# Optimization experiments

Hardware: AMD Instinct MI355X
Metric: run time of the kernel (lower is better)

The kernel has to match this reference:

```python
import jax, jax.numpy as jnp
import numpy as np

N, D, O, V, E, C = 100000, 128, 128, 3, 400000, 2

def setup_inputs() -> dict:
    key = jax.random.key(0)
    ks = jax.random.split(key, 32)
    s = 0.05
    inp = {
        'features': jax.random.normal(ks[0], (N, D), jnp.float32),
        'edge_index': jax.random.randint(ks[1], (V, 2, E), 0, N, jnp.int32),
        'edge_weight': jax.random.uniform(ks[2], (V, E), jnp.float32),
        # per-view RelationAggregator (single relation each)
        'rel_w': jax.random.normal(ks[3], (V, D, O)) * s,
        'rel_b': jnp.zeros((V, O)),
        'gate_w': jax.random.normal(ks[4], (V, O, O)) * s,
        'gate_b': jnp.zeros((V, O)),
        # LabelAwareAttention
        'la_w1': jax.random.normal(ks[5], (C, D, D // 2)) * s,
        'la_b1': jnp.zeros((C, D // 2)),
        'la_w2': jax.random.normal(ks[6], (C, D // 2)) * s,
        'la_b2': jnp.zeros((C,)),
        'pred_w': jax.random.normal(ks[7], (D, C)) * s,
        'pred_b': jnp.zeros((C,)),
        'att_bias': jnp.float32(0.1),
        # ViewLevelAttention
        'view_pref': jax.random.normal(ks[8], (V, O)),
        'va_w1': jax.random.normal(ks[9], (O, O // 2)) * s,
        'va_b1': jnp.zeros((O // 2,)),
        'va_w2': jax.random.normal(ks[10], (O // 2,)) * s,
        'va_b2': jnp.float32(0.0),
        # linear heads
        'ft_w': jax.random.normal(ks[11], (D, O)) * s,
        'ft_b': jnp.zeros((O,)),
        'sl_w': jax.random.normal(ks[12], (D, O)) * s,
        'sl_b': jnp.zeros((O,)),
        'fus_w': jax.random.normal(ks[13], (2 * O, O)) * s,
        'fus_b': jnp.zeros((O,)),
        'ln_g': jnp.ones((O,)),
        'ln_beta': jnp.zeros((O,)),
    }
    return inp


def _aggregate_view(features, ei, ew, w, b, gw, gb):
    # gather -> linear -> edge weight -> scatter-add (fused segment_sum)
    msg = (features[ei[0]] @ w + b) * ew[:, None]          # [E, O]
    agg = jax.ops.segment_sum(msg, ei[1], num_segments=N)  # [N, O]
    # relation_weight_net: softmax over 1 relation == 1.0 (identity)
    gate = jax.nn.sigmoid(agg @ gw + gb)
    return gate * agg


def reference(features, edge_index, edge_weight, rel_w, rel_b, gate_w, gate_b,
              la_w1, la_b1, la_w2, la_b2, pred_w, pred_b, att_bias,
              view_pref, va_w1, va_b1, va_w2, va_b2,
              ft_w, ft_b, sl_w, sl_b, fus_w, fus_b, ln_g, ln_beta):
    # --- label-aware attention ---
    class_probs = jax.nn.softmax(features @ pred_w + pred_b, axis=-1)        # [N, C]
    h = jax.nn.relu(jnp.einsum('nd,cdk->nck', features, la_w1) + la_b1)      # [N, C, D/2]
    scores = jax.nn.sigmoid(jnp.einsum('nck,ck->nc', h, la_w2) + la_b2)      # [N, C]
    node_att = jnp.sum(scores * class_probs, axis=-1) + att_bias             # [N]

    # --- per-view relation aggregation ---
    views = jax.vmap(_aggregate_view, in_axes=(None, 0, 0, 0, 0, 0, 0))(
        features, edge_index, edge_weight, rel_w, rel_b, gate_w, gate_b)     # [V, N, O]

    # --- view-level attention ---
    pe = views * view_pref[:, None, :]                                       # [V, N, O]
    vh = jax.nn.relu(jnp.einsum('vno,ok->vnk', pe, va_w1) + va_b1)           # [V, N, O/2]
    vscore = jnp.einsum('vnk,k->vn', vh, va_w2) + va_b2                      # [V, N]
    v_att = jax.nn.softmax(vscore, axis=0)                                   # over views
    combined = jnp.sum(views * v_att[..., None], axis=0)                     # [N, O]

    # --- fusion (dropout in eval mode == identity) ---
    self_out = features @ sl_w + sl_b
    transformed = features @ ft_w + ft_b
    weighted = combined * node_att[:, None]
    fused = jax.nn.relu(jnp.concatenate([self_out, weighted], axis=-1) @ fus_w + fus_b)
    out = fused + transformed

    mu = jnp.mean(out, axis=-1, keepdims=True)
    var = jnp.mean(jnp.square(out - mu), axis=-1, keepdims=True)
    out = (out - mu) / jnp.sqrt(var + 1e-5) * ln_g + ln_beta
    return out, class_probs
```

## Files before the change

### kernel.cpp

```cpp
#include <hip/hip_runtime.h>

#define N_ 100000
#define D_ 128
#define O_ 128
#define V_ 3
#define E_ 400000
#define NB_SCAN 98
#define EGRID 1563
#define MB 32
#define NBLK (N_ / MB)
#define LDA 136

#define PRE_CVT  6250
#define PRE_PREW (PRE_CVT + 64)
#define PRE_PREP (PRE_PREW + 617)
#define PRE_TOT  (PRE_PREP + 3 * EGRID)

typedef unsigned short u16;
typedef __attribute__((ext_vector_type(8))) short bf16x8;
typedef __attribute__((ext_vector_type(4))) float f32x4;

#define MFMA16x16x32 __builtin_amdgcn_mfma_f32_16x16x32_bf16

#define P_RELB  0
#define P_GATEB 384
#define P_VP    768
#define P_VAB1  1152
#define P_VAW2  1216
#define P_VAB2  1280
#define P_LAB1  1281
#define P_LAW2  1409
#define P_LAB2  1537
#define P_PREDB 1539
#define P_ATTB  1541
#define P_FTB   1542
#define P_LNG   1670
#define P_LNB   1798
#define P_PREDW 1926
#define P_TOTAL 2182

__device__ __forceinline__ float b2f(u16 u) {
    union { float f; unsigned int i; } x; x.i = ((unsigned int)u) << 16; return x.f;
}
__device__ __forceinline__ float blo(unsigned int u) {
    union { float f; unsigned int i; } x; x.i = u << 16; return x.f;
}
__device__ __forceinline__ float bhi(unsigned int u) {
    union { float f; unsigned int i; } x; x.i = u & 0xffff0000u; return x.f;
}
__device__ __forceinline__ u16 f2b(float f) {
    union { float f; unsigned int i; } x; x.f = f;
    unsigned int r = x.i + 0x7FFFu + ((x.i >> 16) & 1u);
    return (u16)(r >> 16);
}

template<int F32> __device__ __forceinline__ float LD(const void* p, size_t i) {
    if (F32) return ((const float*)p)[i];
    return b2f(((const u16*)p)[i]);
}

__global__ void k_detect(const u16* __restrict__ feat, int* __restrict__ flag) {
    int t = threadIdx.x;
    u16 a = feat[2 * t], b = feat[2 * t + 128];
    int zeros = (a == 0 ? 1 : 0) + (b == 0 ? 1 : 0);
    float va = b2f(a), vb = b2f(b);
    int bad = (!(va > -128.f && va < 128.f) ? 1 : 0) +
              (!(vb > -128.f && vb < 128.f) ? 1 : 0);
    #pragma unroll
    for (int s = 1; s <= 32; s <<= 1) {
        bad += __shfl_xor(bad, s);
        zeros += __shfl_xor(zeros, s);
    }
    if (t == 0) flag[0] = (bad >= 16 || zeros >= 64) ? 1 : 0;
}

__device__ __forceinline__ void cvt_body_f32(int b, const void* feat,
                                             u16* __restrict__ featB) {
    size_t idx = (size_t)b * 256 + threadIdx.x;
    const float4* fp = (const float4*)feat;
    float4 a = fp[idx * 2], c = fp[idx * 2 + 1];
    uint4 u;
    u.x = (unsigned)f2b(a.x) | ((unsigned)f2b(a.y) << 16);
    u.y = (unsigned)f2b(a.z) | ((unsigned)f2b(a.w) << 16);
    u.z = (unsigned)f2b(c.x) | ((unsigned)f2b(c.y) << 16);
    u.w = (unsigned)f2b(c.z) | ((unsigned)f2b(c.w) << 16);
    ((uint4*)featB)[idx] = u;
}

template<int F32>
__device__ __forceinline__ void prew_body(int b, const void* sl_w, const void* sl_b,
                                          const void* fus_w, const void* fus_b,
                                          u16* __restrict__ W1T, float* __restrict__ b1) {
    int gid = b * 256 + threadIdx.x;
    int d = gid >> 7, o = gid & 127;
    float acc = 0.f;
    for (int k = 0; k < 128; ++k)
        acc += LD<F32>(sl_w, d * 128 + k) * LD<F32>(fus_w, k * 128 + o);
    W1T[o * 128 + d] = f2b(acc);
    if (gid < 128) {
        float accb = 0.f;
        for (int k = 0; k < 128; ++k)
            accb += LD<F32>(sl_b, k) * LD<F32>(fus_w, k * 128 + gid);
        b1[gid] = accb + LD<F32>(fus_b, gid);
    }
}

template<int F32>
__device__ __forceinline__ void prep_body(int b,
        const void* rel_w, const void* gate_w, const void* va_w1, const void* fus_w,
        const void* ft_w, const void* la_w1,
        const void* rel_b, const void* gate_b, const void* vpref,
        const void* va_b1, const void* va_w2, const void* va_b2,
        const void* la_b1, const void* la_w2, const void* la_b2,
        const void* pred_b, const void* att_bias, const void* ft_b,
        const void* ln_g, const void* ln_beta, const void* pred_w,
        u16* __restrict__ relT, u16* __restrict__ gateT, u16* __restrict__ vaT,
        u16* __restrict__ fus2T, u16* __restrict__ ftT, u16* __restrict__ laT,
        float* __restrict__ P) {
    int id = b * 256 + threadIdx.x;
    if (id < 49152) {
        int v = id >> 14, r = id & 16383, o = r >> 7, d = r & 127;
        relT[id] = f2b(LD<F32>(rel_w, (size_t)v * 16384 + d * 128 + o));
    } else if (id < 98304) {
        int t = id - 49152, v = t >> 14, r = t & 16383, o = r >> 7, d = r & 127;
        gateT[t] = f2b(LD<F32>(gate_w, (size_t)v * 16384 + d * 128 + o));
    } else if (id < 106496) {
        int t = id - 98304, n = t >> 7, k = t & 127;
        vaT[t] = f2b(LD<F32>(va_w1, k * 64 + n));
    } else if (id < 122880) {
        int t = id - 106496, n = t >> 7, k = t & 127;
        fus2T[t] = f2b(LD<F32>(fus_w, (128 + k) * 128 + n));
    } else if (id < 139264) {
        int t = id - 122880, o = t >> 7, d = t & 127;
        ftT[t] = f2b(LD<F32>(ft_w, d * 128 + o));
    } else if (id < 155648) {
        int t = id - 139264, n = t >> 7, d = t & 127;
        int c = n >> 6, j = n & 63;
        laT[t] = f2b(LD<F32>(la_w1, c * 8192 + d * 64 + j));
    } else if (id < 155648 + P_TOTAL) {
        int t = id - 155648;
        float val;
        if      (t < P_GATEB) val = LD<F32>(rel_b, t);
        else if (t < P_VP)    val = LD<F32>(gate_b, t - P_GATEB);
        else if (t < P_VAB1)  val = LD<F32>(vpref, t - P_VP);
        else if (t < P_VAW2)  val = LD<F32>(va_b1, t - P_VAB1);
        else if (t < P_VAB2)  val = LD<F32>(va_w2, t - P_VAW2);
        else if (t < P_LAB1)  val = LD<F32>(va_b2, 0);
        else if (t < P_LAW2)  val = LD<F32>(la_b1, t - P_LAB1);
        else if (t < P_LAB2)  val = LD<F32>(la_w2, t - P_LAW2);
        else if (t < P_PREDB) val = LD<F32>(la_b2, t - P_LAB2);
        else if (t < P_ATTB)  val = LD<F32>(pred_b, t - P_PREDB);
        else if (t < P_FTB)   val = LD<F32>(att_bias, 0);
        else if (t < P_LNG)   val = LD<F32>(ft_b, t - P_FTB);
        else if (t < P_LNB)   val = LD<F32>(ln_g, t - P_LNG);
        else if (t < P_PREDW) val = LD<F32>(ln_beta, t - P_LNB);
        else                  val = LD<F32>(pred_w, t - P_PREDW);
        P[t] = val;
    }
}

__global__ __launch_bounds__(256) void k_preC(const int* __restrict__ flag,
        const void* feat, u16* __restrict__ featB,
        const void* sl_w, const void* sl_b, const void* fus_w, const void* fus_b,
        u16* __restrict__ W1T, float* __restrict__ b1,
        const void* rel_w, const void* gate_w, const void* va_w1,
        const void* ft_w, const void* la_w1,
        const void* rel_b, const void* gate_b, const void* vpref,
        const void* va_b1, const void* va_w2, const void* va_b2,
        const void* la_b1, const void* la_w2, const void* la_b2,
        const void* pred_b, const void* att_bias, const void* ft_b,
        const void* ln_g, const void* ln_beta, const void* pred_w,
        u16* __restrict__ relT, u16* __restrict__ gateT, u16* __restrict__ vaT,
        u16* __restrict__ fus2T, u16* __restrict__ ftT, u16* __restrict__ laT,
        float* __restrict__ P,
        const int* __restrict__ ei, int* __restrict__ cur3) {
    int b = blockIdx.x;
    if (b < PRE_CVT) {
        if (flag[0]) cvt_body_f32(b, feat, featB);
    } else if (b < PRE_PREW) {
        if (flag[0]) prew_body<1>(b - PRE_CVT, sl_w, sl_b, fus_w, fus_b, W1T, b1);
        else         prew_body<0>(b - PRE_CVT, sl_w, sl_b, fus_w, fus_b, W1T, b1);
    } else if (b < PRE_PREP) {
        if (flag[0]) prep_body<1>(b - PRE_PREW, rel_w, gate_w, va_w1, fus_w, ft_w, la_w1,
                                  rel_b, gate_b, vpref, va_b1, va_w2, va_b2,
                                  la_b1, la_w2, la_b2, pred_b, att_bias, ft_b,
                                  ln_g, ln_beta, pred_w, relT, gateT, vaT, fus2T, ftT, laT, P);
        else         prep_body<0>(b - PRE_PREW, rel_w, gate_w, va_w1, fus_w, ft_w, la_w1,
                                  rel_b, gate_b, vpref, va_b1, va_w2, va_b2,
                                  la_b1, la_w2, la_b2, pred_b, att_bias, ft_b,
                                  ln_g, ln_beta, pred_w, relT, gateT, vaT, fus2T, ftT, laT, P);
    } else {
        int b2 = b - PRE_PREP;
        int v = b2 / EGRID;
        int e = (b2 % EGRID) * 256 + threadIdx.x;
        if (e < E_) atomicAdd(&cur3[v * N_ + ei[(size_t)v * 2 * E_ + E_ + e]], 1);
    }
}

__global__ __launch_bounds__(256) void k_scan_bsum(const int* __restrict__ cur3,
                                                   int* __restrict__ bsum) {
    __shared__ int red[256];
    const int v = blockIdx.x / NB_SCAN, b = blockIdx.x % NB_SCAN, tid = threadIdx.x;
    const int base = b * 1024;
    const int* counts = cur3 + v * N_;
    int s = 0;
    for (int i = tid; i < 1024; i += 256) {
        int idx = base + i;
        s += (idx < N_) ? counts[idx] : 0;
    }
    red[tid] = s;
    __syncthreads();
    for (int st = 128; st >= 1; st >>= 1) {
        if (tid < st) red[tid] += red[tid + st];
        __syncthreads();
    }
    if (tid == 0) bsum[v * 128 + b] = red[0];
}

__global__ __launch_bounds__(256) void k_scan_write(int* __restrict__ cur3,
                                                    const int* __restrict__ bsum,
                                                    int* __restrict__ offs3) {
    __shared__ int lsum[256];
    __shared__ int bs_s[128];
    const int v = blockIdx.x / NB_SCAN, b = blockIdx.x % NB_SCAN, tid = threadIdx.x;
    const int base = b * 1024;
    int* counts = cur3 + v * N_;
    int* offs   = offs3 + v * N_;
    if (tid < 128) bs_s[tid] = (tid < b) ? bsum[v * 128 + tid] : 0;
    int c[4]; int s = 0;
    #pragma unroll
    for (int k = 0; k < 4; ++k) {
        int idx = base + tid * 4 + k;
        c[k] = (idx < N_) ? counts[idx] : 0;
        s += c[k];
    }
    lsum[tid] = s;
    __syncthreads();
    for (int st = 1; st < 256; st <<= 1) {
        int t = (tid >= st) ? lsum[tid - st] : 0;
        __syncthreads();
        lsum[tid] += t;
        __syncthreads();
    }
    for (int st = 64; st >= 1; st >>= 1) {
        if (tid < st) bs_s[tid] += bs_s[tid + st];
        __syncthreads();
    }
    int off = bs_s[0] + lsum[tid] - s;
    #pragma unroll
    for (int k = 0; k < 4; ++k) {
        int idx = base + tid * 4 + k;
        if (idx < N_) { offs[idx] = off; counts[idx] = off; }
        off += c[k];
    }
}

template<int F32>
__device__ __forceinline__ void place_body(const int* __restrict__ ei, const void* ew_all,
                                           int* __restrict__ cur3, int2* __restrict__ srcw3) {
    int v = blockIdx.x / EGRID;
    int e = (blockIdx.x % EGRID) * 256 + threadIdx.x;
    if (e < E_) {
        int dst = ei[(size_t)v * 2 * E_ + E_ + e];
        int src = ei[(size_t)v * 2 * E_ + e];
        float w = LD<F32>(ew_all, (size_t)v * E_ + e);
        int pos = atomicAdd(&cur3[v * N_ + dst], 1);
        int2 sw; sw.x = src; sw.y = __float_as_int(w);
        srcw3[(size_t)v * E_ + pos] = sw;
    }
}
__global__ __launch_bounds__(256) void k_place(const int* __restrict__ flag,
                                               const int* __restrict__ ei, const void* ew,
                                               int* __restrict__ cur3, int2* __restrict__ srcw3) {
    if (flag[0]) place_body<1>(ei, ew, cur3, srcw3);
    else         place_body<0>(ei, ew, cur3, srcw3);
}

__global__ __launch_bounds__(768, 6) void k_fused(const int* __restrict__ flag,
        const void* feat, const u16* __restrict__ featB_,
        const int2* __restrict__ srcw3,
        const int* __restrict__ offs3, const int* __restrict__ ends3,
        const u16* __restrict__ relT, const u16* __restrict__ gateT,
        const u16* __restrict__ vaT, const u16* __restrict__ W1T,
        const u16* __restrict__ fus2T, const u16* __restrict__ ftT,
        const u16* __restrict__ laT,
        const float* __restrict__ b1, const float* __restrict__ P,
        void* __restrict__ d_out) {
    const int f32 = flag[0];
    const u16* __restrict__ fb = f32 ? featB_ : (const u16*)feat;

    __shared__ __align__(16) u16 xA[MB * LDA];
    __shared__ __align__(16) u16 zbuf[3][MB * LDA];
    __shared__ __align__(16) float Fbuf[MB * 128];
    __shared__ float vp3_s[3][128];
    __shared__ float redL[4][MB];
    __shared__ float redv[3][4][MB];
    __shared__ float wsn3[3][MB];
    __shared__ float aw_s[MB][3];
    __shared__ float natt_s[MB];
    __shared__ float lg_s[MB][2];
    __shared__ float mrs_s[MB][2];
    __shared__ float vab1_s[64], vaw2_s[64];
    __shared__ float predw_s[256];
    __shared__ float b1_s[128], ftb_s[128], lng_s[128], lnb_s[128];

    const int tid = threadIdx.x;
    const int g   = tid >> 8;
    const int t256 = tid & 255;
    const int wid = t256 >> 6;
    const int L = t256 & 63, q = L >> 4, i = L & 15;
    const int nb = wid * 32;
    const int nodebase = blockIdx.x * MB;
    const int nl = t256 >> 5, l32 = t256 & 31, o4 = l32 * 4;
    const int gsub = t256 >> 4, l16 = tid & 15, o8 = l16 * 8;
    const f32x4 zz = {0.f, 0.f, 0.f, 0.f};

    auto ldf = [&](const u16* B, int row, int k0) -> bf16x8 {
        return *(const bf16x8*)&B[row * LDA + k0];
    };
    auto ldg = [&](const u16* B, int row, int k0) -> bf16x8 {
        return *(const bf16x8*)&B[row * 128 + k0];
    };
    auto gemm32 = [&](const u16* A, const u16* Bg, f32x4 acc[2][2]) {
        #pragma unroll
        for (int kk = 0; kk < 4; ++kk) {
            int k0 = q * 8 + kk * 32;
            bf16x8 a0 = ldf(A, i, k0);
            bf16x8 a1 = ldf(A, i + 16, k0);
            bf16x8 bb0 = ldg(Bg, nb + i, k0);
            bf16x8 bb1 = ldg(Bg, nb + 16 + i, k0);
            acc[0][0] = MFMA16x16x32(a0, bb0, acc[0][0], 0, 0, 0);
            acc[0][1] = MFMA16x16x32(a0, bb1, acc[0][1], 0, 0, 0);
            acc[1][0] = MFMA16x16x32(a1, bb0, acc[1][0], 0, 0, 0);
            acc[1][1] = MFMA16x16x32(a1, bb1, acc[1][1], 0, 0, 0);
        }
    };
    auto gather = [&]() {
        const int* offs = offs3 + g * N_;
        const int* ends = ends3 + g * N_;
        const int2* srcw = srcw3 + (size_t)g * E_;
        #pragma unroll
        for (int rep = 0; rep < 2; ++rep) {
            const int m = gsub + rep * 16;
            const int node = nodebase + m;
            float z0 = 0.f, z1 = 0.f, z2 = 0.f, z3 = 0.f;
            float z4 = 0.f, z5 = 0.f, z6 = 0.f, z7 = 0.f, ws = 0.f;
            int j = offs[node], jend = ends[node];
            while (j < jend) {
                int r = jend - j;
                int2 e0 = srcw[j];
                int2 e1, e2, e3;
                e1.x = 0; e1.y = 0; e2.x = 0; e2.y = 0; e3.x = 0; e3.y = 0;
                if (r > 1) e1 = srcw[j + 1];
                if (r > 2) e2 = srcw[j + 2];
                if (r > 3) e3 = srcw[j + 3];
                uint4 x0, x1, x2, x3;
                x1.x = x1.y = x1.z = x1.w = 0;
                x2.x = x2.y = x2.z = x2.w = 0;
                x3.x = x3.y = x3.z = x3.w = 0;
                x0 = *(const uint4*)&fb[(size_t)e0.x * 128 + o8];
                if (r > 1) x1 = *(const uint4*)&fb[(size_t)e1.x * 128 + o8];
                if (r > 2) x2 = *(const uint4*)&fb[(size_t)e2.x * 128 + o8];
                if (r > 3) x3 = *(const uint4*)&fb[(size_t)e3.x * 128 + o8];
                float w0 = __int_as_float(e0.y), w1 = __int_as_float(e1.y);
                float w2 = __int_as_float(e2.y), w3 = __int_as_float(e3.y);
                ws += w0 + w1 + w2 + w3;
                z0 += w0 * blo(x0.x) + w1 * blo(x1.x) + w2 * blo(x2.x) + w3 * blo(x3.x);
                z1 += w0 * bhi(x0.x) + w1 * bhi(x1.x) + w2 * bhi(x2.x) + w3 * bhi(x3.x);
                z2 += w0 * blo(x0.y) + w1 * blo(x1.y) + w2 * blo(x2.y) + w3 * blo(x3.y);
                z3 += w0 * bhi(x0.y) + w1 * bhi(x1.y) + w2 * bhi(x2.y) + w3 * bhi(x3.y);
                z4 += w0 * blo(x0.z) + w1 * blo(x1.z) + w2 * blo(x2.z) + w3 * blo(x3.z);
                z5 += w0 * bhi(x0.z) + w1 * bhi(x1.z) + w2 * bhi(x2.z) + w3 * bhi(x3.z);
                z6 += w0 * blo(x0.w) + w1 * blo(x1.w) + w2 * blo(x2.w) + w3 * blo(x3.w);
                z7 += w0 * bhi(x0.w) + w1 * bhi(x1.w) + w2 * bhi(x2.w) + w3 * bhi(x3.w);
                j += 4;
            }
            uint4 u;
            u.x = (unsigned)f2b(z0) | ((unsigned)f2b(z1) << 16);
            u.y = (unsigned)f2b(z2) | ((unsigned)f2b(z3) << 16);
            u.z = (unsigned)f2b(z4) | ((unsigned)f2b(z5) << 16);
            u.w = (unsigned)f2b(z6) | ((unsigned)f2b(z7) << 16);
            *(uint4*)&zbuf[g][m * LDA + o8] = u;
            if (l16 == 0) wsn3[g][m] = ws;
        }
    };

    if (tid < 512) {
        int m = tid >> 4, s = tid & 15;
        *(uint4*)&xA[m * LDA + s * 8] =
            *(const uint4*)&fb[(size_t)(nodebase + m) * 128 + s * 8];
    }
    if (tid < 64) { vab1_s[tid] = P[P_VAB1 + tid]; vaw2_s[tid] = P[P_VAW2 + tid]; }
    if (tid < 128) {
        b1_s[tid]  = b1[tid];
        ftb_s[tid] = P[P_FTB + tid];
        lng_s[tid] = P[P_LNG + tid];
        lnb_s[tid] = P[P_LNB + tid];
    }
    if (tid < 256) predw_s[tid] = P[P_PREDW + tid];
    if (tid >= 256 && tid < 640) {
        int t = tid - 256;
        vp3_s[t >> 7][t & 127] = P[P_VP + t];
    }
    gather();
    __syncthreads();

    f32x4 accA[2][2] = {{zz, zz}, {zz, zz}};
    gemm32(zbuf[g], relT + (size_t)g * 16384, accA);
    if (g == 0) {
        f32x4 accL[2][2] = {{zz, zz}, {zz, zz}};
        gemm32(xA, laT, accL);
        #pragma unroll
        for (int rep = 0; rep < 4; ++rep) {
            int m = rep * 8 + nl;
            float lg0 = 0.f, lg1 = 0.f;
            #pragma unroll
            for (int t = 0; t < 4; ++t) {
                float xv = b2f(xA[m * LDA + o4 + t]);
                lg0 += xv * predw_s[(o4 + t) * 2 + 0];
                lg1 += xv * predw_s[(o4 + t) * 2 + 1];
            }
            #pragma unroll
            for (int s = 1; s <= 16; s <<= 1) {
                lg0 += __shfl_xor(lg0, s);
                lg1 += __shfl_xor(lg1, s);
            }
            if (l32 == 0) { lg_s[m][0] = lg0; lg_s[m][1] = lg1; }
        }
        float la0 = P[P_LAB1 + nb + i],  la1 = P[P_LAB1 + nb + 16 + i];
        float lw0 = P[P_LAW2 + nb + i],  lw1 = P[P_LAW2 + nb + 16 + i];
        float partL[2][4];
        #pragma unroll
        for (int mt = 0; mt < 2; ++mt)
            #pragma unroll
            for (int r = 0; r < 4; ++r) {
                float h0 = fmaxf(accL[mt][0][r] + la0, 0.f);
                float h1 = fmaxf(accL[mt][1][r] + la1, 0.f);
                partL[mt][r] = h0 * lw0 + h1 * lw1;
            }
        #pragma unroll
        for (int s = 1; s <= 8; s <<= 1)
            #pragma unroll
            for (int mt = 0; mt < 2; ++mt)
                #pragma unroll
                for (int r = 0; r < 4; ++r)
                    partL[mt][r] += __shfl_xor(partL[mt][r], s);
        if (i == 0)
            #pragma unroll
            for (int mt = 0; mt < 2; ++mt)
                #pragma unroll
                for (int r = 0; r < 4; ++r)
                    redL[wid][mt * 16 + q * 4 + r] = partL[mt][r];
    }
    __syncthreads();

    {
        float rb0 = P[P_RELB + g * 128 + nb + i];
        float rb1 = P[P_RELB + g * 128 + nb + 16 + i];
        #pragma unroll
        for (int mt = 0; mt < 2; ++mt)
            #pragma unroll
            for (int nt = 0; nt < 2; ++nt) {
                float rb = nt ? rb1 : rb0;
                int col = nb + nt * 16 + i;
                #pragma unroll
                for (int r = 0; r < 4; ++r) {
                    int row = mt * 16 + q * 4 + r;
                    float a = accA[mt][nt][r] + wsn3[g][row] * rb;
                    accA[mt][nt][r] = a;
                    zbuf[g][row * LDA + col] = f2b(a);
                }
            }
    }
    if (tid < MB) {
        float c0 = redL[0][tid] + redL[1][tid] + P[P_LAB2 + 0];
        float c1 = redL[2][tid] + redL[3][tid] + P[P_LAB2 + 1];
        float s0 = 1.f / (1.f + __expf(-c0));
        float s1 = 1.f / (1.f + __expf(-c1));
        float l0 = lg_s[tid][0] + P[P_PREDB + 0];
        float l1 = lg_s[tid][1] + P[P_PREDB + 1];
        float mx = fmaxf(l0, l1);
        float e0 = __expf(l0 - mx), e1 = __expf(l1 - mx);
        float inv = 1.f / (e0 + e1);
        float p0 = e0 * inv, p1 = e1 * inv;
        natt_s[tid] = s0 * p0 + s1 * p1 + P[P_ATTB];
        int node = nodebase + tid;
        if (f32) {
            float* pr = (float*)d_out + (size_t)N_ * O_;
            pr[node * 2 + 0] = p0; pr[node * 2 + 1] = p1;
        } else {
            u16* pr = (u16*)d_out + (size_t)N_ * O_;
            pr[node * 2 + 0] = f2b(p0); pr[node * 2 + 1] = f2b(p1);
        }
    }
    __syncthreads();

    f32x4 acc2[2][2] = {{zz, zz}, {zz, zz}};
    gemm32(zbuf[g], gateT + (size_t)g * 16384, acc2);
    __syncthreads();

    {
        float gb0 = P[P_GATEB + g * 128 + nb + i];
        float gb1 = P[P_GATEB + g * 128 + nb + 16 + i];
        #pragma unroll
        for (int mt = 0; mt < 2; ++mt)
            #pragma unroll
            for (int nt = 0; nt < 2; ++nt) {
                float gb = nt ? gb1 : gb0;
                int col = nb + nt * 16 + i;
                #pragma unroll
                for (int r = 0; r < 4; ++r) {
                    int row = mt * 16 + q * 4 + r;
                    float gt = 1.f / (1.f + __expf(-(acc2[mt][nt][r] + gb)));
                    zbuf[g][row * LDA + col] = f2b(gt * accA[mt][nt][r]);
                }
            }
    }
    __syncthreads();

    {
        f32x4 accV[2] = {zz, zz};
        const int nbv = wid * 16, colv = nbv + i;
        #pragma unroll
        for (int kk = 0; kk < 4; ++kk) {
            int k0 = q * 8 + kk * 32;
            bf16x8 a0r = ldf(zbuf[g], i, k0);
            bf16x8 a1r = ldf(zbuf[g], i + 16, k0);
            bf16x8 a0, a1;
            #pragma unroll
            for (int e = 0; e < 8; ++e) {
                float vp = vp3_s[g][k0 + e];
                a0[e] = (short)f2b(b2f((u16)a0r[e]) * vp);
                a1[e] = (short)f2b(b2f((u16)a1r[e]) * vp);
            }
            bf16x8 bb = ldg(vaT, nbv + i, k0);
            accV[0] = MFMA16x16x32(a0, bb, accV[0], 0, 0, 0);
            accV[1] = MFMA16x16x32(a1, bb, accV[1], 0, 0, 0);
        }
        float part[2][4];
        #pragma unroll
        for (int mt = 0; mt < 2; ++mt)
            #pragma unroll
            for (int r = 0; r < 4; ++r) {
                float vh = fmaxf(accV[mt][r] + vab1_s[colv], 0.f);
                part[mt][r] = vh * vaw2_s[colv];
            }
        #pragma unroll
        for (int s = 1; s <= 8; s <<= 1)
            #pragma unroll
            for (int mt = 0; mt < 2; ++mt)
                #pragma unroll
                for (int r = 0; r < 4; ++r)
                    part[mt][r] += __shfl_xor(part[mt][r], s);
        if (i == 0)
            #pragma unroll
            for (int mt = 0; mt < 2; ++mt)
                #pragma unroll
                for (int r = 0; r < 4; ++r)
                    redv[g][wid][mt * 16 + q * 4 + r] = part[mt][r];
    }
    __syncthreads();

    if (tid < MB) {
        float sv[3];
        #pragma unroll
        for (int v = 0; v < 3; ++v)
            sv[v] = redv[v][0][tid] + redv[v][1][tid] +
                    redv[v][2][tid] + redv[v][3][tid] + P[P_VAB2];
        float mx = fmaxf(sv[0], fmaxf(sv[1], sv[2]));
        float e0 = __expf(sv[0] - mx), e1 = __expf(sv[1] - mx), e2 = __expf(sv[2] - mx);
        float inv = natt_s[tid] / (e0 + e1 + e2);
        aw_s[tid][0] = e0 * inv; aw_s[tid][1] = e1 * inv; aw_s[tid][2] = e2 * inv;
    }
    __syncthreads();

    for (int idx = tid; idx < MB * 128; idx += 768) {
        int row = idx >> 7, col = idx & 127;
        float w = aw_s[row][0] * b2f(zbuf[0][row * LDA + col]) +
                  aw_s[row][1] * b2f(zbuf[1][row * LDA + col]) +
                  aw_s[row][2] * b2f(zbuf[2][row * LDA + col]);
        zbuf[0][row * LDA + col] = f2b(w);
    }
    __syncthreads();

    float* F1 = (float*)&zbuf[1][0];
    f32x4 accG[2][2] = {{zz, zz}, {zz, zz}};
    if (g == 0) {
        gemm32(xA, W1T, accG);
        #pragma unroll
        for (int mt = 0; mt < 2; ++mt)
            #pragma unroll
            for (int nt = 0; nt < 2; ++nt)
                #pragma unroll
                for (int r = 0; r < 4; ++r)
                    F1[(mt * 16 + q * 4 + r) * 128 + nb + nt * 16 + i] = accG[mt][nt][r];
    } else if (g == 1) {
        gemm32(zbuf[0], fus2T, accG);
        #pragma unroll
        for (int mt = 0; mt < 2; ++mt)
            #pragma unroll
            for (int nt = 0; nt < 2; ++nt)
                #pragma unroll
                for (int r = 0; r < 4; ++r)
                    Fbuf[(mt * 16 + q * 4 + r) * 128 + nb + nt * 16 + i] = accG[mt][nt][r];
    } else {
        gemm32(xA, ftT, accG);
    }
    __syncthreads();

    float ov[2][2][4];
    if (g == 2) {
        float ps[2][4], pq[2][4];
        #pragma unroll
        for (int mt = 0; mt < 2; ++mt)
            #pragma unroll
            for (int r = 0; r < 4; ++r) { ps[mt][r] = 0.f; pq[mt][r] = 0.f; }
        #pragma unroll
        for (int mt = 0; mt < 2; ++mt)
            #pragma unroll
            for (int nt = 0; nt < 2; ++nt)
                #pragma unroll
                for (int r = 0; r < 4; ++r) {
                    int row = mt * 16 + q * 4 + r, col = nb + nt * 16 + i;
                    float o = fmaxf(F1[row * 128 + col] + Fbuf[row * 128 + col]
                                    + b1_s[col], 0.f)
                              + accG[mt][nt][r] + ftb_s[col];
                    ov[mt][nt][r] = o;
                    ps[mt][r] += o; pq[mt][r] += o * o;
                }
        #pragma unroll
        for (int s = 1; s <= 8; s <<= 1)
            #pragma unroll
            for (int mt = 0; mt < 2; ++mt)
                #pragma unroll
                for (int r = 0; r < 4; ++r) {
                    ps[mt][r] += __shfl_xor(ps[mt][r], s);
                    pq[mt][r] += __shfl_xor(pq[mt][r], s);
                }
        float* red2 = &redv[0][0][0];
        if (i == 0)
            #pragma unroll
            for (int mt = 0; mt < 2; ++mt)
                #pragma unroll
                for (int r = 0; r < 4; ++r) {
                    int row = mt * 16 + q * 4 + r;
                    red2[wid * 64 + row * 2 + 0] = ps[mt][r];
                    red2[wid * 64 + row * 2 + 1] = pq[mt][r];
                }
    }
    __syncthreads();

    if (tid < MB) {
        const float* red2 = &redv[0][0][0];
        float sm = red2[tid * 2] + red2[64 + tid * 2] +
                   red2[128 + tid * 2] + red2[192 + tid * 2];
        float sq = red2[tid * 2 + 1] + red2[64 + tid * 2 + 1] +
                   red2[128 + tid * 2 + 1] + red2[192 + tid * 2 + 1];
        float mu = sm * (1.f / 128.f);
        float var = sq * (1.f / 128.f) - mu * mu;
        mrs_s[tid][0] = mu; mrs_s[tid][1] = rsqrtf(var + 1e-5f);
    }
    __syncthreads();

    if (g == 2) {
        #pragma unroll
        for (int mt = 0; mt < 2; ++mt)
            #pragma unroll
            for (int nt = 0; nt < 2; ++nt)
                #pragma unroll
                for (int r = 0; r < 4; ++r) {
                    int row = mt * 16 + q * 4 + r, col = nb + nt * 16 + i;
                    float val = (ov[mt][nt][r] - mrs_s[row][0]) * mrs_s[row][1]
                                * lng_s[col] + lnb_s[col];
                    if (f32) Fbuf[row * 128 + col] = val;
                    else     ((u16*)Fbuf)[row * 128 + col] = f2b(val);
                }
    }
    __syncthreads();

    if (f32) {
        float* op = (float*)d_out + (size_t)nodebase * 128;
        for (int idx = tid; idx < 1024; idx += 768)
            ((float4*)op)[idx] = ((const float4*)Fbuf)[idx];
    } else {
        u16* op = (u16*)d_out + (size_t)nodebase * 128;
        if (tid < 512)
            ((uint4*)op)[tid] = ((const uint4*)Fbuf)[tid];
    }
}

extern "C" void kernel_launch(void* const* d_in, const int* in_sizes, int n_in,
                              void* d_out, int out_size, void* d_ws, size_t ws_size,
                              hipStream_t stream) {
    const void* feat     = d_in[0];
    const int*  ei       = (const int*)d_in[1];
    const void* ew       = d_in[2];
    const void* rel_w    = d_in[3];
    const void* rel_b    = d_in[4];
    const void* gate_w   = d_in[5];
    const void* gate_b   = d_in[6];
    const void* la_w1    = d_in[7];
    const void* la_b1    = d_in[8];
    const void* la_w2    = d_in[9];
    const void* la_b2    = d_in[10];
    const void* pred_w   = d_in[11];
    const void* pred_b   = d_in[12];
    const void* att_bias = d_in[13];
    const void* view_pref= d_in[14];
    const void* va_w1    = d_in[15];
    const void* va_b1    = d_in[16];
    const void* va_w2    = d_in[17];
    const void* va_b2    = d_in[18];
    const void* ft_w     = d_in[19];
    const void* ft_b     = d_in[20];
    const void* sl_w     = d_in[21];
    const void* sl_b     = d_in[22];
    const void* fus_w    = d_in[23];
    const void* fus_b    = d_in[24];
    const void* ln_g     = d_in[25];
    const void* ln_beta  = d_in[26];

    int*   flag  = (int*)d_ws;
    int*   offs3 = flag + 4;
    int*   cur3  = offs3 + 3 * N_;
    int2*  srcw3 = (int2*)(cur3 + 3 * N_);
    int*   bsum  = (int*)(srcw3 + 3 * E_);
    float* b1    = (float*)(bsum + 3 * 128);
    float* P     = b1 + 128;
    u16*   W1T   = (u16*)(P + 2304);
    u16*   relT  = W1T + 16384;
    u16*   gateT = relT + 3 * 16384;
    u16*   vaT   = gateT + 3 * 16384;
    u16*   fus2T = vaT + 8192;
    u16*   ftT   = fus2T + 16384;
    u16*   laT   = ftT + 16384;
    u16*   featB = laT + 16384;

    k_detect<<<1, 64, 0, stream>>>((const u16*)feat, flag);
    (void)hipMemsetAsync(cur3, 0, 3 * N_ * sizeof(int), stream);
    k_preC<<<PRE_TOT, 256, 0, stream>>>(flag, feat, featB,
                                        sl_w, sl_b, fus_w, fus_b, W1T, b1,
                                        rel_w, gate_w, va_w1, ft_w, la_w1,
                                        rel_b, gate_b, view_pref,
                                        va_b1, va_w2, va_b2,
                                        la_b1, la_w2, la_b2,
                                        pred_b, att_bias, ft_b, ln_g, ln_beta, pred_w,
                                        relT, gateT, vaT, fus2T, ftT, laT, P,
                                        ei, cur3);
    k_scan_bsum<<<3 * NB_SCAN, 256, 0, stream>>>(cur3, bsum);
    k_scan_write<<<3 * NB_SCAN, 256, 0, stream>>>(cur3, bsum, offs3);
    k_place<<<3 * EGRID, 256, 0, stream>>>(flag, ei, ew, cur3, srcw3);
    k_fused<<<NBLK, 768, 0, stream>>>(flag, feat, featB, srcw3, offs3, cur3,
                                      relT, gateT, vaT, W1T, fus2T, ftT, laT,
                                      b1, P, d_out);
}
```

Before: 544.2 us.

## Double node tile to 64 per block with aliased shared-memory buffers

Raises the fused kernel's node tile from 32 to 64, so each weight B-fragment loaded from global memory feeds four MFMA row tiles instead of two, halving per-node weight traffic. To fit the larger tile, the separate xA/zbuf/Fbuf shared arrays become one aliased buffer, several small parameter arrays are read straight from global memory, and LayerNorm is applied during the output store. Bounds checks handle the partial last block. This raises register pressure and shared-memory size per block, which may cut occupancy, especially with launch bounds still at (768,6).

New measurement: 610.6 us. 1.12x slower.

```diff
diff --git a/kernel.cpp b/kernel.cpp
--- a/kernel.cpp
+++ b/kernel.cpp
@@ -7,8 +7,8 @@
 #define E_ 400000
 #define NB_SCAN 98
 #define EGRID 1563
-#define MB 32
-#define NBLK (N_ / MB)
+#define MB 64
+#define NBLK 1563
 #define LDA 136
 
 #define PRE_CVT  6250
@@ -289,9 +289,7 @@
     const int f32 = flag[0];
     const u16* __restrict__ fb = f32 ? featB_ : (const u16*)feat;
 
-    __shared__ __align__(16) u16 xA[MB * LDA];
-    __shared__ __align__(16) u16 zbuf[3][MB * LDA];
-    __shared__ __align__(16) float Fbuf[MB * 128];
+    __shared__ __align__(16) u16 S[4 * MB * LDA];
     __shared__ float vp3_s[3][128];
     __shared__ float redL[4][MB];
     __shared__ float redv[3][4][MB];
@@ -300,9 +298,11 @@
     __shared__ float natt_s[MB];
     __shared__ float lg_s[MB][2];
     __shared__ float mrs_s[MB][2];
-    __shared__ float vab1_s[64], vaw2_s[64];
-    __shared__ float predw_s[256];
-    __shared__ float b1_s[128], ftb_s[128], lng_s[128], lnb_s[128];
+
+    u16* xA = S;
+    float* F1 = (float*)(S + 2 * MB * LDA);
+    float* F2 = (float*)S;
+    float* red2 = &redv[0][0][0];
 
     const int tid = threadIdx.x;
     const int g   = tid >> 8;
@@ -314,6 +314,7 @@
     const int nl = t256 >> 5, l32 = t256 & 31, o4 = l32 * 4;
     const int gsub = t256 >> 4, l16 = tid & 15, o8 = l16 * 8;
     const f32x4 zz = {0.f, 0.f, 0.f, 0.f};
+    u16* zc = S + (size_t)(1 + g) * MB * LDA;
 
     auto ldf = [&](const u16* B, int row, int k0) -> bf16x8 {
         return *(const bf16x8*)&B[row * LDA + k0];
@@ -321,18 +322,18 @@
     auto ldg = [&](const u16* B, int row, int k0) -> bf16x8 {
         return *(const bf16x8*)&B[row * 128 + k0];
     };
-    auto gemm32 = [&](const u16* A, const u16* Bg, f32x4 acc[2][2]) {
+    auto gemm64 = [&](const u16* A, const u16* Bg, f32x4 acc[4][2]) {
         #pragma unroll
         for (int kk = 0; kk < 4; ++kk) {
             int k0 = q * 8 + kk * 32;
-            bf16x8 a0 = ldf(A, i, k0);
-            bf16x8 a1 = ldf(A, i + 16, k0);
             bf16x8 bb0 = ldg(Bg, nb + i, k0);
             bf16x8 bb1 = ldg(Bg, nb + 16 + i, k0);
-            acc[0][0] = MFMA16x16x32(a0, bb0, acc[0][0], 0, 0, 0);
-            acc[0][1] = MFMA16x16x32(a0, bb1, acc[0][1], 0, 0, 0);
-            acc[1][0] = MFMA16x16x32(a1, bb0, acc[1][0], 0, 0, 0);
-            acc[1][1] = MFMA16x16x32(a1, bb1, acc[1][1], 0, 0, 0);
+            #pragma unroll
+            for (int mt = 0; mt < 4; ++mt) {
+                bf16x8 a = ldf(A, i + mt * 16, k0);
+                acc[mt][0] = MFMA16x16x32(a, bb0, acc[mt][0], 0, 0, 0);
+                acc[mt][1] = MFMA16x16x32(a, bb1, acc[mt][1], 0, 0, 0);
+            }
         }
     };
     auto gather = [&]() {
@@ -340,64 +341,60 @@
         const int* ends = ends3 + g * N_;
         const int2* srcw = srcw3 + (size_t)g * E_;
         #pragma unroll
-        for (int rep = 0; rep < 2; ++rep) {
+        for (int rep = 0; rep < 4; ++rep) {
             const int m = gsub + rep * 16;
             const int node = nodebase + m;
-            float z0 = 0.f, z1 = 0.f, z2 = 0.f, z3 = 0.f;
-            float z4 = 0.f, z5 = 0.f, z6 = 0.f, z7 = 0.f, ws = 0.f;
-            int j = offs[node], jend = ends[node];
-            while (j < jend) {
-                int r = jend - j;
-                int2 e0 = srcw[j];
-                int2 e1, e2, e3;
-                e1.x = 0; e1.y = 0; e2.x = 0; e2.y = 0; e3.x = 0; e3.y = 0;
-                if (r > 1) e1 = srcw[j + 1];
-                if (r > 2) e2 = srcw[j + 2];
-                if (r > 3) e3 = srcw[j + 3];
-                uint4 x0, x1, x2, x3;
-                x1.x = x1.y = x1.z = x1.w = 0;
-                x2.x = x2.y = x2.z = x2.w = 0;
-                x3.x = x3.y = x3.z = x3.w = 0;
-                x0 = *(const uint4*)&fb[(size_t)e0.x * 128 + o8];
-                if (r > 1) x1 = *(const uint4*)&fb[(size_t)e1.x * 128 + o8];
-                if (r > 2) x2 = *(const uint4*)&fb[(size_t)e2.x * 128 + o8];
-                if (r > 3) x3 = *(const uint4*)&fb[(size_t)e3.x * 128 + o8];
-                float w0 = __int_as_float(e0.y), w1 = __int_as_float(e1.y);
-                float w2 = __int_as_float(e2.y), w3 = __int_as_float(e3.y);
-                ws += w0 + w1 + w2 + w3;
-                z0 += w0 * blo(x0.x) + w1 * blo(x1.x) + w2 * blo(x2.x) + w3 * blo(x3.x);
-                z1 += w0 * bhi(x0.x) + w1 * bhi(x1.x) + w2 * bhi(x2.x) + w3 * bhi(x3.x);
-                z2 += w0 * blo(x0.y) + w1 * blo(x1.y) + w2 * blo(x2.y) + w3 * blo(x3.y);
-                z3 += w0 * bhi(x0.y) + w1 * bhi(x1.y) + w2 * bhi(x2.y) + w3 * bhi(x3.y);
-                z4 += w0 * blo(x0.z) + w1 * blo(x1.z) + w2 * blo(x2.z) + w3 * blo(x3.z);
-                z5 += w0 * bhi(x0.z) + w1 * bhi(x1.z) + w2 * bhi(x2.z) + w3 * bhi(x3.z);
-                z6 += w0 * blo(x0.w) + w1 * blo(x1.w) + w2 * blo(x2.w) + w3 * blo(x3.w);
-                z7 += w0 * bhi(x0.w) + w1 * bhi(x1.w) + w2 * bhi(x2.w) + w3 * bhi(x3.w);
-                j += 4;
-            }
-            uint4 u;
-            u.x = (unsigned)f2b(z0) | ((unsigned)f2b(z1) << 16);
-            u.y = (unsigned)f2b(z2) | ((unsigned)f2b(z3) << 16);
-            u.z = (unsigned)f2b(z4) | ((unsigned)f2b(z5) << 16);
-            u.w = (unsigned)f2b(z6) | ((unsigned)f2b(z7) << 16);
-            *(uint4*)&zbuf[g][m * LDA + o8] = u;
-            if (l16 == 0) wsn3[g][m] = ws;
+            if (node < N_) {
+                float z0 = 0.f, z1 = 0.f, z2 = 0.f, z3 = 0.f;
+                float z4 = 0.f, z5 = 0.f, z6 = 0.f, z7 = 0.f, ws = 0.f;
+                int j = offs[node], jend = ends[node];
+                while (j < jend) {
+                    int r = jend - j;
+                    int2 e0 = srcw[j];
+                    int2 e1, e2, e3;
+                    e1.x = 0; e1.y = 0; e2.x = 0; e2.y = 0; e3.x = 0; e3.y = 0;
+                    if (r > 1) e1 = srcw[j + 1];
+                    if (r > 2) e2 = srcw[j + 2];
+                    if (r > 3) e3 = srcw[j + 3];
+                    uint4 x0, x1, x2, x3;
+                    x1.x = x1.y = x1.z = x1.w = 0;
+                    x2.x = x2.y = x2.z = x2.w = 0;
+                    x3.x = x3.y = x3.z = x3.w = 0;
+                    x0 = *(const uint4*)&fb[(size_t)e0.x * 128 + o8];
+                    if (r > 1) x1 = *(const uint4*)&fb[(size_t)e1.x * 128 + o8];
+                    if (r > 2) x2 = *(const uint4*)&fb[(size_t)e2.x * 128 + o8];
+                    if (r > 3) x3 = *(const uint4*)&fb[(size_t)e3.x * 128 + o8];
+                    float w0 = __int_as_float(e0.y), w1 = __int_as_float(e1.y);
+                    float w2 = __int_as_float(e2.y), w3 = __int_as_float(e3.y);
+                    ws += w0 + w1 + w2 + w3;
+                    z0 += w0 * blo(x0.x) + w1 * blo(x1.x) + w2 * blo(x2.x) + w3 * blo(x3.x);
+                    z1 += w0 * bhi(x0.x) + w1 * bhi(x1.x) + w2 * bhi(x2.x) + w3 * bhi(x3.x);
+                    z2 += w0 * blo(x0.y) + w1 * blo(x1.y) + w2 * blo(x2.y) + w3 * blo(x3.y);
+                    z3 += w0 * bhi(x0.y) + w1 * bhi(x1.y) + w2 * bhi(x2.y) + w3 * bhi(x3.y);
+                    z4 += w0 * blo(x0.z) + w1 * blo(x1.z) + w2 * blo(x2.z) + w3 * blo(x3.z);
+                    z5 += w0 * bhi(x0.z) + w1 * bhi(x1.z) + w2 * bhi(x2.z) + w3 * bhi(x3.z);
+                    z6 += w0 * blo(x0.w) + w1 * blo(x1.w) + w2 * blo(x2.w) + w3 * blo(x3.w);
+                    z7 += w0 * bhi(x0.w) + w1 * bhi(x1.w) + w2 * bhi(x2.w) + w3 * bhi(x3.w);
+                    j += 4;
+                }
+                uint4 u;
+                u.x = (unsigned)f2b(z0) | ((unsigned)f2b(z1) << 16);
+                u.y = (unsigned)f2b(z2) | ((unsigned)f2b(z3) << 16);
+                u.z = (unsigned)f2b(z4) | ((unsigned)f2b(z5) << 16);
+                u.w = (unsigned)f2b(z6) | ((unsigned)f2b(z7) << 16);
+                *(uint4*)&zc[m * LDA + o8] = u;
+                if (l16 == 0) wsn3[g][m] = ws;
+            }
         }
     };
 
-    if (tid < 512) {
-        int m = tid >> 4, s = tid & 15;
-        *(uint4*)&xA[m * LDA + s * 8] =
-            *(const uint4*)&fb[(size_t)(nodebase + m) * 128 + s * 8];
-    }
-    if (tid < 64) { vab1_s[tid] = P[P_VAB1 + tid]; vaw2_s[tid] = P[P_VAW2 + tid]; }
-    if (tid < 128) {
-        b1_s[tid]  = b1[tid];
-        ftb_s[tid] = P[P_FTB + tid];
-        lng_s[tid] = P[P_LNG + tid];
-        lnb_s[tid] = P[P_LNB + tid];
-    }
-    if (tid < 256) predw_s[tid] = P[P_PREDW + tid];
+    for (int idx = tid; idx < MB * 16; idx += 768) {
+        int m = idx >> 4, s = idx & 15;
+        int node = nodebase + m;
+        uint4 u; u.x = 0; u.y = 0; u.z = 0; u.w = 0;
+        if (node < N_) u = *(const uint4*)&fb[(size_t)node * 128 + s * 8];
+        *(uint4*)&xA[m * LDA + s * 8] = u;
+    }
     if (tid >= 256 && tid < 640) {
         int t = tid - 256;
         vp3_s[t >> 7][t & 127] = P[P_VP + t];
@@ -405,20 +402,24 @@
     gather();
     __syncthreads();
 
-    f32x4 accA[2][2] = {{zz, zz}, {zz, zz}};
-    gemm32(zbuf[g], relT + (size_t)g * 16384, accA);
     if (g == 0) {
-        f32x4 accL[2][2] = {{zz, zz}, {zz, zz}};
-        gemm32(xA, laT, accL);
-        #pragma unroll
-        for (int rep = 0; rep < 4; ++rep) {
+        f32x4 accL[4][2] = {{zz, zz}, {zz, zz}, {zz, zz}, {zz, zz}};
+        gemm64(xA, laT, accL);
+        float pw[8];
+        #pragma unroll
+        for (int t = 0; t < 4; ++t) {
+            pw[2 * t]     = P[P_PREDW + (o4 + t) * 2];
+            pw[2 * t + 1] = P[P_PREDW + (o4 + t) * 2 + 1];
+        }
+        #pragma unroll
+        for (int rep = 0; rep < 8; ++rep) {
             int m = rep * 8 + nl;
             float lg0 = 0.f, lg1 = 0.f;
             #pragma unroll
             for (int t = 0; t < 4; ++t) {
                 float xv = b2f(xA[m * LDA + o4 + t]);
-                lg0 += xv * predw_s[(o4 + t) * 2 + 0];
-                lg1 += xv * predw_s[(o4 + t) * 2 + 1];
+                lg0 += xv * pw[2 * t];
+                lg1 += xv * pw[2 * t + 1];
             }
             #pragma unroll
             for (int s = 1; s <= 16; s <<= 1) {
@@ -429,36 +430,35 @@
         }
         float la0 = P[P_LAB1 + nb + i],  la1 = P[P_LAB1 + nb + 16 + i];
         float lw0 = P[P_LAW2 + nb + i],  lw1 = P[P_LAW2 + nb + 16 + i];
-        float partL[2][4];
-        #pragma unroll
-        for (int mt = 0; mt < 2; ++mt)
+        #pragma unroll
+        for (int mt = 0; mt < 4; ++mt) {
+            float partL[4];
             #pragma unroll
             for (int r = 0; r < 4; ++r) {
                 float h0 = fmaxf(accL[mt][0][r] + la0, 0.f);
                 float h1 = fmaxf(accL[mt][1][r] + la1, 0.f);
-                partL[mt][r] = h0 * lw0 + h1 * lw1;
-            }
-        #pragma unroll
-        for (int s = 1; s <= 8; s <<= 1)
-            #pragma unroll
-            for (int mt = 0; mt < 2; ++mt)
+                partL[r] = h0 * lw0 + h1 * lw1;
+            }
+            #pragma unroll
+            for (int s = 1; s <= 8; s <<= 1)
                 #pragma unroll
                 for (int r = 0; r < 4; ++r)
-                    partL[mt][r] += __shfl_xor(partL[mt][r], s);
-        if (i == 0)
-            #pragma unroll
-            for (int mt = 0; mt < 2; ++mt)
+                    partL[r] += __shfl_xor(partL[r], s);
+            if (i == 0)
                 #pragma unroll
                 for (int r = 0; r < 4; ++r)
-                    redL[wid][mt * 16 + q * 4 + r] = partL[mt][r];
-    }
+                    redL[wid][mt * 16 + q * 4 + r] = partL[r];
+        }
+    }
+    f32x4 accA[4][2] = {{zz, zz}, {zz, zz}, {zz, zz}, {zz, zz}};
+    gemm64(zc, relT + (size_t)g * 16384, accA);
     __syncthreads();
 
     {
         float rb0 = P[P_RELB + g * 128 + nb + i];
         float rb1 = P[P_RELB + g * 128 + nb + 16 + i];
         #pragma unroll
-        for (int mt = 0; mt < 2; ++mt)
+        for (int mt = 0; mt < 4; ++mt)
             #pragma unroll
             for (int nt = 0; nt < 2; ++nt) {
                 float rb = nt ? rb1 : rb0;
@@ -468,7 +468,7 @@
                     int row = mt * 16 + q * 4 + r;
                     float a = accA[mt][nt][r] + wsn3[g][row] * rb;
                     accA[mt][nt][r] = a;
-                    zbuf[g][row * LDA + col] = f2b(a);
+                    zc[row * LDA + col] = f2b(a);
                 }
             }
     }
@@ -485,25 +485,27 @@
         float p0 = e0 * inv, p1 = e1 * inv;
         natt_s[tid] = s0 * p0 + s1 * p1 + P[P_ATTB];
         int node = nodebase + tid;
-        if (f32) {
-            float* pr = (float*)d_out + (size_t)N_ * O_;
-            pr[node * 2 + 0] = p0; pr[node * 2 + 1] = p1;
-        } else {
-            u16* pr = (u16*)d_out + (size_t)N_ * O_;
-            pr[node * 2 + 0] = f2b(p0); pr[node * 2 + 1] = f2b(p1);
-        }
-    }
-    __syncthreads();
-
-    f32x4 acc2[2][2] = {{zz, zz}, {zz, zz}};
-    gemm32(zbuf[g], gateT + (size_t)g * 16384, acc2);
+        if (node < N_) {
+            if (f32) {
+                float* pr = (float*)d_out + (size_t)N_ * O_;
+                pr[node * 2 + 0] = p0; pr[node * 2 + 1] = p1;
+            } else {
+                u16* pr = (u16*)d_out + (size_t)N_ * O_;
+                pr[node * 2 + 0] = f2b(p0); pr[node * 2 + 1] = f2b(p1);
+            }
+        }
+    }
+    __syncthreads();
+
+    f32x4 acc2[4][2] = {{zz, zz}, {zz, zz}, {zz, zz}, {zz, zz}};
+    gemm64(zc, gateT + (size_t)g * 16384, acc2);
     __syncthreads();
 
     {
         float gb0 = P[P_GATEB + g * 128 + nb + i];
         float gb1 = P[P_GATEB + g * 128 + nb + 16 + i];
         #pragma unroll
-        for (int mt = 0; mt < 2; ++mt)
+        for (int mt = 0; mt < 4; ++mt)
             #pragma unroll
             for (int nt = 0; nt < 2; ++nt) {
                 float gb = nt ? gb1 : gb0;
@@ -512,52 +514,48 @@
                 for (int r = 0; r < 4; ++r) {
                     int row = mt * 16 + q * 4 + r;
                     float gt = 1.f / (1.f + __expf(-(acc2[mt][nt][r] + gb)));
-                    zbuf[g][row * LDA + col] = f2b(gt * accA[mt][nt][r]);
+                    zc[row * LDA + col] = f2b(gt * accA[mt][nt][r]);
                 }
             }
     }
     __syncthreads();
 
     {
-        f32x4 accV[2] = {zz, zz};
+        f32x4 accV[4] = {zz, zz, zz, zz};
         const int nbv = wid * 16, colv = nbv + i;
         #pragma unroll
         for (int kk = 0; kk < 4; ++kk) {
             int k0 = q * 8 + kk * 32;
-            bf16x8 a0r = ldf(zbuf[g], i, k0);
-            bf16x8 a1r = ldf(zbuf[g], i + 16, k0);
-            bf16x8 a0, a1;
-            #pragma unroll
-            for (int e = 0; e < 8; ++e) {
-                float vp = vp3_s[g][k0 + e];
-                a0[e] = (short)f2b(b2f((u16)a0r[e]) * vp);
-                a1[e] = (short)f2b(b2f((u16)a1r[e]) * vp);
-            }
             bf16x8 bb = ldg(vaT, nbv + i, k0);
-            accV[0] = MFMA16x16x32(a0, bb, accV[0], 0, 0, 0);
-            accV[1] = MFMA16x16x32(a1, bb, accV[1], 0, 0, 0);
-        }
-        float part[2][4];
-        #pragma unroll
-        for (int mt = 0; mt < 2; ++mt)
+            #pragma unroll
+            for (int mt = 0; mt < 4; ++mt) {
+                bf16x8 ar = ldf(zc, i + mt * 16, k0);
+                bf16x8 a;
+                #pragma unroll
+                for (int e = 0; e < 8; ++e)
+                    a[e] = (short)f2b(b2f((u16)ar[e]) * vp3_s[g][k0 + e]);
+                accV[mt] = MFMA16x16x32(a, bb, accV[mt], 0, 0, 0);
+            }
+        }
+        float vb1v = P[P_VAB1 + colv], vw2v = P[P_VAW2 + colv];
+        #pragma unroll
+        for (int mt = 0; mt < 4; ++mt) {
+            float part[4];
             #pragma unroll
             for (int r = 0; r < 4; ++r) {
-                float vh = fmaxf(accV[mt][r] + vab1_s[colv], 0.f);
-                part[mt][r] = vh * vaw2_s[colv];
-            }
-        #pragma unroll
-        for (int s = 1; s <= 8; s <<= 1)
-            #pragma unroll
-            for (int mt = 0; mt < 2; ++mt)
+                float vh = fmaxf(accV[mt][r] + vb1v, 0.f);
+                part[r] = vh * vw2v;
+            }
+            #pragma unroll
+            for (int s = 1; s <= 8; s <<= 1)
                 #pragma unroll
                 for (int r = 0; r < 4; ++r)
-                    part[mt][r] += __shfl_xor(part[mt][r], s);
-        if (i == 0)
-            #pragma unroll
-            for (int mt = 0; mt < 2; ++mt)
+                    part[r] += __shfl_xor(part[r], s);
+            if (i == 0)
                 #pragma unroll
                 for (int r = 0; r < 4; ++r)
-                    redv[g][wid][mt * 16 + q * 4 + r] = part[mt][r];
+                    redv[g][wid][mt * 16 + q * 4 + r] = part[r];
+        }
     }
     __syncthreads();
 
@@ -574,118 +572,118 @@
     }
     __syncthreads();
 
-    for (int idx = tid; idx < MB * 128; idx += 768) {
-        int row = idx >> 7, col = idx & 127;
-        float w = aw_s[row][0] * b2f(zbuf[0][row * LDA + col]) +
-                  aw_s[row][1] * b2f(zbuf[1][row * LDA + col]) +
-                  aw_s[row][2] * b2f(zbuf[2][row * LDA + col]);
-        zbuf[0][row * LDA + col] = f2b(w);
-    }
-    __syncthreads();
-
-    float* F1 = (float*)&zbuf[1][0];
-    f32x4 accG[2][2] = {{zz, zz}, {zz, zz}};
+    {
+        u16* z0p = S + MB * LDA;
+        u16* z1p = S + 2 * MB * LDA;
+        u16* z2p = S + 3 * MB * LDA;
+        for (int idx = tid; idx < MB * 128; idx += 768) {
+            int row = idx >> 7, col = idx & 127;
+            float w = aw_s[row][0] * b2f(z0p[row * LDA + col]) +
+                      aw_s[row][1] * b2f(z1p[row * LDA + col]) +
+                      aw_s[row][2] * b2f(z2p[row * LDA + col]);
+            z0p[row * LDA + col] = f2b(w);
+        }
+    }
+    __syncthreads();
+
+    f32x4 accG[4][2] = {{zz, zz}, {zz, zz}, {zz, zz}, {zz, zz}};
     if (g == 0) {
-        gemm32(xA, W1T, accG);
-        #pragma unroll
-        for (int mt = 0; mt < 2; ++mt)
+        gemm64(xA, W1T, accG);
+        #pragma unroll
+        for (int mt = 0; mt < 4; ++mt)
             #pragma unroll
             for (int nt = 0; nt < 2; ++nt)
                 #pragma unroll
                 for (int r = 0; r < 4; ++r)
                     F1[(mt * 16 + q * 4 + r) * 128 + nb + nt * 16 + i] = accG[mt][nt][r];
     } else if (g == 1) {
-        gemm32(zbuf[0], fus2T, accG);
-        #pragma unroll
-        for (int mt = 0; mt < 2; ++mt)
+        gemm64(S + MB * LDA, fus2T, accG);
+    } else {
+        gemm64(xA, ftT, accG);
+    }
+    __syncthreads();
+    if (g == 1) {
+        #pragma unroll
+        for (int mt = 0; mt < 4; ++mt)
             #pragma unroll
             for (int nt = 0; nt < 2; ++nt)
                 #pragma unroll
                 for (int r = 0; r < 4; ++r)
-                    Fbuf[(mt * 16 + q * 4 + r) * 128 + nb + nt * 16 + i] = accG[mt][nt][r];
-    } else {
-        gemm32(xA, ftT, accG);
-    }
-    __syncthreads();
-
-    float ov[2][2][4];
+                    F2[(mt * 16 + q * 4 + r) * 128 + nb + nt * 16 + i] = accG[mt][nt][r];
+    }
+    __syncthreads();
+
     if (g == 2) {
-        float ps[2][4], pq[2][4];
-        #pragma unroll
-        for (int mt = 0; mt < 2; ++mt)
-            #pragma unroll
-            for (int r = 0; r < 4; ++r) { ps[mt][r] = 0.f; pq[mt][r] = 0.f; }
-        #pragma unroll
-        for (int mt = 0; mt < 2; ++mt)
-            #pragma unroll
-            for (int nt = 0; nt < 2; ++nt)
+        float b1v0 = b1[nb + i], b1v1 = b1[nb + 16 + i];
+        float fb0 = P[P_FTB + nb + i], fb1 = P[P_FTB + nb + 16 + i];
+        #pragma unroll
+        for (int mt = 0; mt < 4; ++mt) {
+            float ps[4] = {0.f, 0.f, 0.f, 0.f}, pq[4] = {0.f, 0.f, 0.f, 0.f};
+            #pragma unroll
+            for (int nt = 0; nt < 2; ++nt) {
+                int col = nb + nt * 16 + i;
+                float bv = nt ? b1v1 : b1v0;
+                float fv = nt ? fb1 : fb0;
                 #pragma unroll
                 for (int r = 0; r < 4; ++r) {
-                    int row = mt * 16 + q * 4 + r, col = nb + nt * 16 + i;
-                    float o = fmaxf(F1[row * 128 + col] + Fbuf[row * 128 + col]
-                                    + b1_s[col], 0.f)
-                              + accG[mt][nt][r] + ftb_s[col];
-                    ov[mt][nt][r] = o;
-                    ps[mt][r] += o; pq[mt][r] += o * o;
+                    int rc = (mt * 16 + q * 4 + r) * 128 + col;
+                    float o = fmaxf(F1[rc] + F2[rc] + bv, 0.f) + accG[mt][nt][r] + fv;
+                    F1[rc] = o;
+                    ps[r] += o; pq[r] += o * o;
                 }
-        #pragma unroll
-        for (int s = 1; s <= 8; s <<= 1)
-            #pragma unroll
-            for (int mt = 0; mt < 2; ++mt)
+            }
+            #pragma unroll
+            for (int s = 1; s <= 8; s <<= 1)
                 #pragma unroll
                 for (int r = 0; r < 4; ++r) {
-                    ps[mt][r] += __shfl_xor(ps[mt][r], s);
-                    pq[mt][r] += __shfl_xor(pq[mt][r], s);
+                    ps[r] += __shfl_xor(ps[r], s);
+                    pq[r] += __shfl_xor(pq[r], s);
                 }
-        float* red2 = &redv[0][0][0];
-        if (i == 0)
-            #pragma unroll
-            for (int mt = 0; mt < 2; ++mt)
+            if (i == 0)
                 #pragma unroll
                 for (int r = 0; r < 4; ++r) {
                     int row = mt * 16 + q * 4 + r;
-                    red2[wid * 64 + row * 2 + 0] = ps[mt][r];
-                    red2[wid * 64 + row * 2 + 1] = pq[mt][r];
+                    red2[(wid * MB + row) * 2 + 0] = ps[r];
+                    red2[(wid * MB + row) * 2 + 1] = pq[r];
                 }
+        }
     }
     __syncthreads();
 
     if (tid < MB) {
-        const float* red2 = &redv[0][0][0];
-        float sm = red2[tid * 2] + red2[64 + tid * 2] +
-                   red2[128 + tid * 2] + red2[192 + tid * 2];
-        float sq = red2[tid * 2 + 1] + red2[64 + tid * 2 + 1] +
-                   red2[128 + tid * 2 + 1] + red2[192 + tid * 2 + 1];
+        float sm = red2[tid * 2]            + red2[(MB + tid) * 2] +
+                   red2[(2 * MB + tid) * 2] + red2[(3 * MB + tid) * 2];
+        float sq = red2[tid * 2 + 1]            + red2[(MB + tid) * 2 + 1] +
+                   red2[(2 * MB + tid) * 2 + 1] + red2[(3 * MB + tid) * 2 + 1];
         float mu = sm * (1.f / 128.f);
         float var = sq * (1.f / 128.f) - mu * mu;
         mrs_s[tid][0] = mu; mrs_s[tid][1] = rsqrtf(var + 1e-5f);
     }
     __syncthreads();
 
-    if (g == 2) {
-        #pragma unroll
-        for (int mt = 0; mt < 2; ++mt)
-            #pragma unroll
-            for (int nt = 0; nt < 2; ++nt)
-                #pragma unroll
-                for (int r = 0; r < 4; ++r) {
-                    int row = mt * 16 + q * 4 + r, col = nb + nt * 16 + i;
-                    float val = (ov[mt][nt][r] - mrs_s[row][0]) * mrs_s[row][1]
-                                * lng_s[col] + lnb_s[col];
-                    if (f32) Fbuf[row * 128 + col] = val;
-                    else     ((u16*)Fbuf)[row * 128 + col] = f2b(val);
-                }
-    }
-    __syncthreads();
-
     if (f32) {
         float* op = (float*)d_out + (size_t)nodebase * 128;
-        for (int idx = tid; idx < 1024; idx += 768)
-            ((float4*)op)[idx] = ((const float4*)Fbuf)[idx];
+        for (int idx = tid; idx < MB * 128; idx += 768) {
+            int row = idx >> 7;
+            if (nodebase + row < N_) {
+                int col = idx & 127;
+                float val = (F1[idx] - mrs_s[row][0]) * mrs_s[row][1]
+                            * P[P_LNG + col] + P[P_LNB + col];
+                op[idx] = val;
+            }
+        }
     } else {
-        u16* op = (u16*)d_out + (size_t)nodebase * 128;
-        if (tid < 512)
-            ((uint4*)op)[tid] = ((const uint4*)Fbuf)[tid];
+        unsigned* op = (unsigned*)d_out + (size_t)nodebase * 64;
+        for (int idx = tid; idx < MB * 64; idx += 768) {
+            int row = idx >> 6;
+            if (nodebase + row < N_) {
+                int c2 = (idx & 63) * 2;
+                float m0 = mrs_s[row][0], r0 = mrs_s[row][1];
+                float v0 = (F1[row * 128 + c2]     - m0) * r0 * P[P_LNG + c2]     + P[P_LNB + c2];
+                float v1 = (F1[row * 128 + c2 + 1] - m0) * r0 * P[P_LNG + c2 + 1] + P[P_LNB + c2 + 1];
+                op[idx] = (unsigned)f2b(v0) | ((unsigned)f2b(v1) << 16);
+            }
+        }
     }
 }
 
```
